# Kernel tuning notes

Hardware: AMD Instinct MI355X
Metric: run time of the kernel (lower is better)

## Reference

```python
import jax, jax.numpy as jnp
import numpy as np

# Static segment boundaries: lengths [512,512,512] + remainder -> ranges below
SEG_RANGES = [(0, 512), (512, 1024), (1024, 1536), (1536, 2048)]

B, N, D, H = 8, 2048, 1024, 2048
NUM_SEG = len(SEG_RANGES)


def setup_inputs() -> dict:
    key = jax.random.key(0)
    k_x, k1, k2, k3 = jax.random.split(key, 4)
    scale_in = 1.0 / np.sqrt(D)
    scale_h = 1.0 / np.sqrt(H)
    return {
        "x": jax.random.normal(k_x, (B, N, D), dtype=jnp.float32),
        "w1": jax.random.normal(k1, (NUM_SEG, D, H), dtype=jnp.float32) * scale_in,
        "w3": jax.random.normal(k2, (NUM_SEG, D, H), dtype=jnp.float32) * scale_in,
        "w2": jax.random.normal(k3, (NUM_SEG, H, D), dtype=jnp.float32) * scale_h,
    }


def reference(x, w1, w3, w2):
    # Per-segment independent SwiGLU FFN: out_seg = (silu(x W1) * (x W3)) W2
    outs = []
    for i, (s, e) in enumerate(SEG_RANGES):
        seg = jax.lax.dynamic_slice_in_dim(x, s, e - s, axis=-2)  # [B, L_i, D]
        h = jax.nn.silu(jnp.einsum('bld,dh->blh', seg, w1[i])) \
            * jnp.einsum('bld,dh->blh', seg, w3[i])               # [B, L_i, H]
        outs.append(jnp.einsum('blh,hd->bld', h, w2[i]))          # [B, L_i, D]
    # Segments tile [0, N) exactly, so concat == the .at[s:e].set() scatter loop
    return jnp.concatenate(outs, axis=-2)
```

## Files before the change

### kernel.cpp

```cpp
#include <hip/hip_runtime.h>
#include <hip/hip_bf16.h>

typedef __bf16 bf16_t;
typedef __attribute__((ext_vector_type(8))) __bf16 bf16x8;
typedef __attribute__((ext_vector_type(4))) float f32x4;
typedef __attribute__((ext_vector_type(8))) unsigned short ushort8v;

#define MFMA16(a, b, c) __builtin_amdgcn_mfma_f32_16x16x32_bf16((a), (b), (c), 0, 0, 0)

__device__ __forceinline__ unsigned short f2bf(float f) {
    bf16_t b = (bf16_t)f;
    return __builtin_bit_cast(unsigned short, b);
}

__device__ __forceinline__ void gload16(const void* g, void* l) {
    __builtin_amdgcn_global_load_lds(
        (const __attribute__((address_space(1))) void*)g,
        (__attribute__((address_space(3))) void*)l,
        16, 0, 0);
}

__global__ __launch_bounds__(256) void cvtx(const float* __restrict__ src,
                                            bf16_t* __restrict__ dst) {
    size_t i = ((size_t)blockIdx.x * 256 + threadIdx.x) * 8;
    f32x4 v0 = *(const f32x4*)(src + i);
    f32x4 v1 = *(const f32x4*)(src + i + 4);
    bf16x8 o;
    o[0] = (bf16_t)v0[0]; o[1] = (bf16_t)v0[1];
    o[2] = (bf16_t)v0[2]; o[3] = (bf16_t)v0[3];
    o[4] = (bf16_t)v1[0]; o[5] = (bf16_t)v1[1];
    o[6] = (bf16_t)v1[2]; o[7] = (bf16_t)v1[3];
    *(bf16x8*)(dst + i) = o;
}

__global__ __launch_bounds__(256) void transcvt64(const float* __restrict__ src,
                                                  unsigned short* __restrict__ dst,
                                                  int R, int C) {
    __shared__ __align__(16) unsigned short tile[64][66];
    size_t off = (size_t)blockIdx.z * R * C;
    const float* s = src + off;
    unsigned short* d = dst + off;
    int tr = blockIdx.y * 64, tc = blockIdx.x * 64;
    int tid = threadIdx.x;
    int lr = tid >> 4;
    int lc = (tid & 15) * 4;
#pragma unroll
    for (int p = 0; p < 4; ++p) {
        int r = p * 16 + lr;
        f32x4 v = *(const f32x4*)(s + (size_t)(tr + r) * C + tc + lc);
        tile[r][lc + 0] = f2bf(v[0]); tile[r][lc + 1] = f2bf(v[1]);
        tile[r][lc + 2] = f2bf(v[2]); tile[r][lc + 3] = f2bf(v[3]);
    }
    __syncthreads();
#pragma unroll
    for (int q = 0; q < 2; ++q) {
        int item = q * 256 + tid;
        int oc = item >> 3;
        int rb = (item & 7) * 8;
        ushort8v v;
#pragma unroll
        for (int t = 0; t < 8; ++t) v[t] = tile[rb + t][oc];
        *(ushort8v*)(d + (size_t)(tc + oc) * R + tr + rb) = v;
    }
}


#define PH_FENCE { __builtin_amdgcn_sched_barrier(0); asm volatile("" ::: "memory"); }
#define LGKM0 { asm volatile("s_waitcnt lgkmcnt(0)" ::: "memory"); __builtin_amdgcn_sched_barrier(0); }

__global__ __launch_bounds__(512, 2) void gemm13(const bf16_t* __restrict__ Xb,
                                                 const bf16_t* __restrict__ W1t,
                                                 const bf16_t* __restrict__ W3t,
                                                 bf16_t* __restrict__ Hh,
                                                 int row_base) {
    const int K = 1024, N = 2048;
    int nwg = gridDim.x, id = blockIdx.x;
    if ((nwg & 7) == 0) id = (id & 7) * (nwg >> 3) + (id >> 3);
    int nbx = nwg >> 4;
    int bx = id % nbx, by = id / nbx;
    int row0 = bx * 256, col0 = by * 128;
    int seg = ((row_base + row0) & 2047) >> 9;
    const bf16_t* Ag  = Xb + (size_t)row0 * K;
    const bf16_t* B1g = W1t + ((size_t)seg * N + col0) * K;
    const bf16_t* B3g = W3t + ((size_t)seg * N + col0) * K;

    __shared__ __align__(16) bf16_t smem[65536];

    int tid = threadIdx.x, lane = tid & 63, w = tid >> 6;
    int wm = w >> 1, wn = w & 1;
    int quad = lane >> 4, l16 = lane & 15;

    int r0 = 2 * (tid >> 3) + ((tid >> 2) & 1);
    int c0 = (tid & 3) ^ ((tid >> 3) & 3);
    int offG  = r0 * K + c0 * 8;
    int offG2 = offG + 128 * K;

    int sigRd = ((l16 & 1) << 2) | (quad ^ ((l16 >> 1) & 3));
    int rdA = (wm * 32 + (l16 >> 1)) * 64 + sigRd * 8;
    int rdB = (wn * 32 + (l16 >> 1)) * 64 + sigRd * 8;

    f32x4 accU[4][4], accV[4][4];
    f32x4 z = {0.f, 0.f, 0.f, 0.f};
#pragma unroll
    for (int i = 0; i < 4; ++i)
#pragma unroll
        for (int j = 0; j < 4; ++j) { accU[i][j] = z; accV[i][j] = z; }

    bf16x8 af[4], bfr[4];

#define STG13(slot, hh) { bf16_t* d_ = smem + (slot) * 16384; const int kg_ = (hh) * 32; \
    gload16(Ag + kg_ + offG,  d_ + tid * 8); \
    gload16(Ag + kg_ + offG2, d_ + 4096 + tid * 8); \
    gload16(B1g + kg_ + offG, d_ + 8192 + tid * 8); \
    gload16(B3g + kg_ + offG, d_ + 12288 + tid * 8); }

#define HALF13(slot, STG, WAIT) {                                               \
    PH_FENCE;                                                                   \
    { const bf16_t* sa_ = smem + (slot) * 16384;                                \
      _Pragma("unroll")                                                         \
      for (int i_ = 0; i_ < 4; ++i_)                                            \
          af[i_] = *(const bf16x8*)(sa_ + rdA + i_ * 512);                      \
      _Pragma("unroll")                                                         \
      for (int j_ = 0; j_ < 4; ++j_)                                            \
          bfr[j_] = *(const bf16x8*)(sa_ + 8192 + rdB + j_ * 512); }            \
    STG;                                                                        \
    __builtin_amdgcn_s_barrier();                                               \
    LGKM0;                                                                      \
    __builtin_amdgcn_s_setprio(1);                                              \
    _Pragma("unroll")                                                           \
    for (int i_ = 0; i_ < 4; ++i_)                                              \
        _Pragma("unroll")                                                       \
        for (int j_ = 0; j_ < 4; ++j_)                                          \
            accU[i_][j_] = MFMA16(af[i_], bfr[j_], accU[i_][j_]);               \
    __builtin_amdgcn_s_setprio(0);                                              \
    __builtin_amdgcn_s_barrier();                                               \
    PH_FENCE;                                                                   \
    { const bf16_t* sb_ = smem + (slot) * 16384 + 12288;                        \
      _Pragma("unroll")                                                         \
      for (int j_ = 0; j_ < 4; ++j_)                                            \
          bfr[j_] = *(const bf16x8*)(sb_ + rdB + j_ * 512); }                   \
    WAIT;                                                                       \
    __builtin_amdgcn_s_barrier();                                               \
    LGKM0;                                                                      \
    __builtin_amdgcn_s_setprio(1);                                              \
    _Pragma("unroll")                                                           \
    for (int i_ = 0; i_ < 4; ++i_)                                              \
        _Pragma("unroll")                                                       \
        for (int j_ = 0; j_ < 4; ++j_)                                          \
            accV[i_][j_] = MFMA16(af[i_], bfr[j_], accV[i_][j_]);               \
    __builtin_amdgcn_s_setprio(0);                                              \
    __builtin_amdgcn_s_barrier(); }

#define W8_13 asm volatile("s_waitcnt vmcnt(8)" ::: "memory")

    STG13(0, 0); STG13(1, 1); STG13(2, 2);
    W8_13;
    __builtin_amdgcn_s_barrier();

#pragma unroll 1
    for (int h = 0; h < 28; h += 4) {
        HALF13(0, STG13(3, h + 3), W8_13);
        HALF13(1, STG13(0, h + 4), W8_13);
        HALF13(2, STG13(1, h + 5), W8_13);
        HALF13(3, STG13(2, h + 6), W8_13);
    }
    HALF13(0, STG13(3, 31), W8_13);
    HALF13(1, , asm volatile("s_waitcnt vmcnt(4)" ::: "memory"));
    HALF13(2, , asm volatile("s_waitcnt vmcnt(0)" ::: "memory"));
    HALF13(3, , );

    __syncthreads();
    bf16_t* Ct = smem;
#pragma unroll
    for (int i = 0; i < 4; ++i)
#pragma unroll
        for (int j = 0; j < 4; ++j) {
            int r = wm * 64 + i * 16 + quad * 4;
            int c = wn * 64 + j * 16 + l16;
#pragma unroll
            for (int t = 0; t < 4; ++t) {
                float u = accU[i][j][t];
                float v = accV[i][j][t];
                float h = (u / (1.f + __expf(-u))) * v;
                Ct[(r + t) * 136 + c] = (bf16_t)h;
            }
        }
    __syncthreads();
#pragma unroll
    for (int s = 0; s < 8; ++s) {
        int r = s * 32 + (tid >> 4);
        int cb = (tid & 15) * 8;
        bf16x8 v = *(const bf16x8*)(Ct + r * 136 + cb);
        *(bf16x8*)(Hh + (size_t)(row0 + r) * N + col0 + cb) = v;
    }
#undef HALF13
#undef STG13
#undef W8_13
}

__global__ __launch_bounds__(512, 2) void gemm2k(const bf16_t* __restrict__ Hh,
                                                 const bf16_t* __restrict__ W2t,
                                                 float* __restrict__ Outc,
                                                 int row_base) {
    const int K = 2048, N = 1024;
    int nwg = gridDim.x, id = blockIdx.x;
    if ((nwg & 7) == 0) id = (id & 7) * (nwg >> 3) + (id >> 3);
    int nbx = nwg >> 2;
    int bx = id % nbx, by = id / nbx;
    int row0 = bx * 256, col0 = by * 256;
    int seg = ((row_base + row0) & 2047) >> 9;
    const bf16_t* Ag = Hh + (size_t)row0 * K;
    const bf16_t* Bg = W2t + ((size_t)seg * N + col0) * K;

    __shared__ __align__(16) bf16_t smem[65536];

    int tid = threadIdx.x, lane = tid & 63, w = tid >> 6;
    int wm = w >> 2, wn = w & 3;
    int quad = lane >> 4, l16 = lane & 15;

    int r0 = 2 * (tid >> 3) + ((tid >> 2) & 1);
    int c0 = (tid & 3) ^ ((tid >> 3) & 3);
    int offG  = r0 * K + c0 * 8;
    int offG2 = offG + 128 * K;

    int sigRd = ((l16 & 1) << 2) | (quad ^ ((l16 >> 1) & 3));
    int rdA = (wm * 64 + (l16 >> 1)) * 64 + sigRd * 8;
    int rdB = (wn * 32 + (l16 >> 1)) * 64 + sigRd * 8;

    f32x4 acc[8][4];
    f32x4 z = {0.f, 0.f, 0.f, 0.f};
#pragma unroll
    for (int i = 0; i < 8; ++i)
#pragma unroll
        for (int j = 0; j < 4; ++j) acc[i][j] = z;

    bf16x8 af[4], bfr[4];

#define STG2(slot, hh) { bf16_t* d_ = smem + (slot) * 16384; const int kg_ = (hh) * 32; \
    gload16(Ag + kg_ + offG,  d_ + tid * 8); \
    gload16(Ag + kg_ + offG2, d_ + 4096 + tid * 8); \
    gload16(Bg + kg_ + offG,  d_ + 8192 + tid * 8); \
    gload16(Bg + kg_ + offG2, d_ + 12288 + tid * 8); }

#define HALF2(slot, STG, WAIT) {                                                \
    PH_FENCE;                                                                   \
    { const bf16_t* s_ = smem + (slot) * 16384;                                 \
      _Pragma("unroll")                                                         \
      for (int i_ = 0; i_ < 4; ++i_)                                            \
          af[i_] = *(const bf16x8*)(s_ + rdA + i_ * 512);                       \
      _Pragma("unroll")                                                         \
      for (int j_ = 0; j_ < 4; ++j_)                                            \
          bfr[j_] = *(const bf16x8*)(s_ + 8192 + rdB + j_ * 512); }             \
    STG;                                                                        \
    __builtin_amdgcn_s_barrier();                                               \
    LGKM0;                                                                      \
    __builtin_amdgcn_s_setprio(1);                                              \
    _Pragma("unroll")                                                           \
    for (int i_ = 0; i_ < 4; ++i_)                                              \
        _Pragma("unroll")                                                       \
        for (int j_ = 0; j_ < 4; ++j_)                                          \
            acc[i_][j_] = MFMA16(af[i_], bfr[j_], acc[i_][j_]);                 \
    __builtin_amdgcn_s_setprio(0);                                              \
    __builtin_amdgcn_s_barrier();                                               \
    PH_FENCE;                                                                   \
    { const bf16_t* s_ = smem + (slot) * 16384;                                 \
      _Pragma("unroll")                                                         \
      for (int i_ = 0; i_ < 4; ++i_)                                            \
          af[i_] = *(const bf16x8*)(s_ + 2048 + rdA + i_ * 512); }              \
    WAIT;                                                                       \
    __builtin_amdgcn_s_barrier();                                               \
    LGKM0;                                                                      \
    __builtin_amdgcn_s_setprio(1);                                              \
    _Pragma("unroll")                                                           \
    for (int i_ = 0; i_ < 4; ++i_)                                              \
        _Pragma("unroll")                                                       \
        for (int j_ = 0; j_ < 4; ++j_)                                          \
            acc[4 + i_][j_] = MFMA16(af[i_], bfr[j_], acc[4 + i_][j_]);         \
    __builtin_amdgcn_s_setprio(0);                                              \
    __builtin_amdgcn_s_barrier(); }

#define W8_2 asm volatile("s_waitcnt vmcnt(8)" ::: "memory")

    STG2(0, 0); STG2(1, 1); STG2(2, 2);
    W8_2;
    __builtin_amdgcn_s_barrier();

#pragma unroll 1
    for (int h = 0; h < 60; h += 4) {
        HALF2(0, STG2(3, h + 3), W8_2);
        HALF2(1, STG2(0, h + 4), W8_2);
        HALF2(2, STG2(1, h + 5), W8_2);
        HALF2(3, STG2(2, h + 6), W8_2);
    }
    HALF2(0, STG2(3, 63), W8_2);
    HALF2(1, , asm volatile("s_waitcnt vmcnt(4)" ::: "memory"));
    HALF2(2, , asm volatile("s_waitcnt vmcnt(0)" ::: "memory"));
    HALF2(3, , );

    __syncthreads();
    float* smemf = (float*)smem;
    for (int pass = 0; pass < 4; ++pass) {
        if (pass) __syncthreads();
        if (wm == (pass >> 1)) {
            int mq = pass & 1;
#pragma unroll
            for (int i = 0; i < 4; ++i)
#pragma unroll
                for (int j = 0; j < 4; ++j) {
                    int r = i * 16 + quad * 4;
                    int c = wn * 64 + j * 16 + l16;
#pragma unroll
                    for (int t = 0; t < 4; ++t)
                        smemf[(r + t) * 260 + c] = acc[mq * 4 + i][j][t];
                }
        }
        __syncthreads();
#pragma unroll
        for (int s = 0; s < 8; ++s) {
            int r = s * 8 + w;
            f32x4 v = *(const f32x4*)(smemf + r * 260 + lane * 4);
            *(f32x4*)(Outc + (size_t)(row0 + pass * 64 + r) * N + col0 + lane * 4) = v;
        }
    }
#undef HALF2
#undef STG2
#undef W8_2
}

extern "C" void kernel_launch(void* const* d_in, const int* in_sizes, int n_in,
                              void* d_out, int out_size, void* d_ws, size_t ws_size,
                              hipStream_t stream) {
    const float* x  = (const float*)d_in[0];
    const float* w1 = (const float*)d_in[1];
    const float* w3 = (const float*)d_in[2];
    const float* w2 = (const float*)d_in[3];
    float* out = (float*)d_out;

    const size_t WSEG = (size_t)4 * 1024 * 2048;
    bf16_t* w1t = (bf16_t*)d_ws;
    bf16_t* w3t = w1t + WSEG;
    bf16_t* w2t = w3t + WSEG;
    bf16_t* dyn = w2t + WSEG;

    transcvt64<<<dim3(32, 16, 4), 256, 0, stream>>>(w1, (unsigned short*)w1t, 1024, 2048);
    transcvt64<<<dim3(32, 16, 4), 256, 0, stream>>>(w3, (unsigned short*)w3t, 1024, 2048);
    transcvt64<<<dim3(16, 32, 4), 256, 0, stream>>>(w2, (unsigned short*)w2t, 2048, 1024);

    const int TOTAL_ROWS = 16384;
    size_t wbytes = 3 * WSEG * sizeof(bf16_t);
    size_t avail = (ws_size > wbytes) ? ws_size - wbytes : 0;
    int chunk_rows = TOTAL_ROWS;
    while (chunk_rows > 256 && (size_t)chunk_rows * 6144 > avail)
        chunk_rows >>= 1;

    for (int rb = 0; rb < TOTAL_ROWS; rb += chunk_rows) {
        bf16_t* Xb = dyn;
        bf16_t* Hh = dyn + (size_t)chunk_rows * 1024;
        cvtx<<<chunk_rows / 2, 256, 0, stream>>>(x + (size_t)rb * 1024, Xb);
        gemm13<<<(chunk_rows / 256) * 16, 512, 0, stream>>>(Xb, w1t, w3t, Hh, rb);
        gemm2k<<<(chunk_rows / 256) * 4, 512, 0, stream>>>(Hh, w2t, out + (size_t)rb * 1024, rb);
    }
}
```

Measured before the change: 397.7 us.

## Issue all LDS fragment reads up front and drop per-half barriers in GEMM loops

In both GEMM kernels, each pipeline stage now issues all twelve fragment reads at once, as inline-asm ds_read_b128 with immediate offsets. It then waits with lgkmcnt(4) before the first MFMA batch and lgkmcnt(0) before the second. The per-half workgroup barriers are collapsed into a single barrier per stage, placed after the vmcnt wait, which removes three barrier round-trips per K-step. The goal is to cut synchronisation stalls and overlap LDS latency with MFMA work. The cost is more live VGPRs for the extra fragment registers, which pressures the 2-waves-per-SIMD occupancy target. Correctness also rests on manual lgkmcnt accounting that the compiler cannot check.

```diff
diff --git a/kernel.cpp b/kernel.cpp
--- a/kernel.cpp
+++ b/kernel.cpp
@@ -7,6 +7,7 @@
 typedef __attribute__((ext_vector_type(8))) unsigned short ushort8v;
 
 #define MFMA16(a, b, c) __builtin_amdgcn_mfma_f32_16x16x32_bf16((a), (b), (c), 0, 0, 0)
+#define BC8(x) __builtin_bit_cast(bf16x8, (x))
 
 __device__ __forceinline__ unsigned short f2bf(float f) {
     bf16_t b = (bf16_t)f;
@@ -65,8 +66,11 @@
 }
 
 
-#define PH_FENCE { __builtin_amdgcn_sched_barrier(0); asm volatile("" ::: "memory"); }
-#define LGKM0 { asm volatile("s_waitcnt lgkmcnt(0)" ::: "memory"); __builtin_amdgcn_sched_barrier(0); }
+#define PH_FENCE __builtin_amdgcn_sched_barrier(0)
+#define LGKMN(n) { asm volatile("s_waitcnt lgkmcnt(" #n ")" ::: "memory"); \
+                   __builtin_amdgcn_sched_barrier(0); }
+#define VMW(n) asm volatile("s_waitcnt vmcnt(" #n ")" ::: "memory")
+#define DSR(dst, a, OFF) asm volatile("ds_read_b128 %0, %1 " OFF : "=v"(dst) : "v"(a))
 
 __global__ __launch_bounds__(512, 2) void gemm13(const bf16_t* __restrict__ Xb,
                                                  const bf16_t* __restrict__ W1t,
@@ -96,8 +100,8 @@
     int offG2 = offG + 128 * K;
 
     int sigRd = ((l16 & 1) << 2) | (quad ^ ((l16 >> 1) & 3));
-    int rdA = (wm * 32 + (l16 >> 1)) * 64 + sigRd * 8;
-    int rdB = (wn * 32 + (l16 >> 1)) * 64 + sigRd * 8;
+    int rdAB = ((wm * 32 + (l16 >> 1)) * 64 + sigRd * 8) * 2;
+    int rdBB = ((wn * 32 + (l16 >> 1)) * 64 + sigRd * 8) * 2;
 
     f32x4 accU[4][4], accV[4][4];
     f32x4 z = {0.f, 0.f, 0.f, 0.f};
@@ -106,7 +110,7 @@
 #pragma unroll
         for (int j = 0; j < 4; ++j) { accU[i][j] = z; accV[i][j] = z; }
 
-    bf16x8 af[4], bfr[4];
+    f32x4 af[4], bU[4], bV[4];
 
 #define STG13(slot, hh) { bf16_t* d_ = smem + (slot) * 16384; const int kg_ = (hh) * 32; \
     gload16(Ag + kg_ + offG,  d_ + tid * 8); \
@@ -116,57 +120,48 @@
 
 #define HALF13(slot, STG, WAIT) {                                               \
     PH_FENCE;                                                                   \
-    { const bf16_t* sa_ = smem + (slot) * 16384;                                \
-      _Pragma("unroll")                                                         \
-      for (int i_ = 0; i_ < 4; ++i_)                                            \
-          af[i_] = *(const bf16x8*)(sa_ + rdA + i_ * 512);                      \
-      _Pragma("unroll")                                                         \
-      for (int j_ = 0; j_ < 4; ++j_)                                            \
-          bfr[j_] = *(const bf16x8*)(sa_ + 8192 + rdB + j_ * 512); }            \
     STG;                                                                        \
-    __builtin_amdgcn_s_barrier();                                               \
-    LGKM0;                                                                      \
+    int aA_ = (slot) * 32768 + rdAB;                                            \
+    int aB_ = (slot) * 32768 + rdBB;                                            \
+    DSR(af[0], aA_, "offset:0");     DSR(af[1], aA_, "offset:1024");            \
+    DSR(af[2], aA_, "offset:2048");  DSR(af[3], aA_, "offset:3072");            \
+    DSR(bU[0], aB_, "offset:16384"); DSR(bU[1], aB_, "offset:17408");           \
+    DSR(bU[2], aB_, "offset:18432"); DSR(bU[3], aB_, "offset:19456");           \
+    DSR(bV[0], aB_, "offset:24576"); DSR(bV[1], aB_, "offset:25600");           \
+    DSR(bV[2], aB_, "offset:26624"); DSR(bV[3], aB_, "offset:27648");           \
+    LGKMN(4);                                                                   \
     __builtin_amdgcn_s_setprio(1);                                              \
     _Pragma("unroll")                                                           \
     for (int i_ = 0; i_ < 4; ++i_)                                              \
         _Pragma("unroll")                                                       \
         for (int j_ = 0; j_ < 4; ++j_)                                          \
-            accU[i_][j_] = MFMA16(af[i_], bfr[j_], accU[i_][j_]);               \
+            accU[i_][j_] = MFMA16(BC8(af[i_]), BC8(bU[j_]), accU[i_][j_]);      \
     __builtin_amdgcn_s_setprio(0);                                              \
-    __builtin_amdgcn_s_barrier();                                               \
-    PH_FENCE;                                                                   \
-    { const bf16_t* sb_ = smem + (slot) * 16384 + 12288;                        \
-      _Pragma("unroll")                                                         \
-      for (int j_ = 0; j_ < 4; ++j_)                                            \
-          bfr[j_] = *(const bf16x8*)(sb_ + rdB + j_ * 512); }                   \
-    WAIT;                                                                       \
-    __builtin_amdgcn_s_barrier();                                               \
-    LGKM0;                                                                      \
+    LGKMN(0);                                                                   \
     __builtin_amdgcn_s_setprio(1);                                              \
     _Pragma("unroll")                                                           \
     for (int i_ = 0; i_ < 4; ++i_)                                              \
         _Pragma("unroll")                                                       \
         for (int j_ = 0; j_ < 4; ++j_)                                          \
-            accV[i_][j_] = MFMA16(af[i_], bfr[j_], accV[i_][j_]);               \
+            accV[i_][j_] = MFMA16(BC8(af[i_]), BC8(bV[j_]), accV[i_][j_]);      \
     __builtin_amdgcn_s_setprio(0);                                              \
+    WAIT;                                                                       \
     __builtin_amdgcn_s_barrier(); }
 
-#define W8_13 asm volatile("s_waitcnt vmcnt(8)" ::: "memory")
-
     STG13(0, 0); STG13(1, 1); STG13(2, 2);
-    W8_13;
+    VMW(8);
     __builtin_amdgcn_s_barrier();
 
 #pragma unroll 1
     for (int h = 0; h < 28; h += 4) {
-        HALF13(0, STG13(3, h + 3), W8_13);
-        HALF13(1, STG13(0, h + 4), W8_13);
-        HALF13(2, STG13(1, h + 5), W8_13);
-        HALF13(3, STG13(2, h + 6), W8_13);
-    }
-    HALF13(0, STG13(3, 31), W8_13);
-    HALF13(1, , asm volatile("s_waitcnt vmcnt(4)" ::: "memory"));
-    HALF13(2, , asm volatile("s_waitcnt vmcnt(0)" ::: "memory"));
+        HALF13(0, STG13(3, h + 3), VMW(8));
+        HALF13(1, STG13(0, h + 4), VMW(8));
+        HALF13(2, STG13(1, h + 5), VMW(8));
+        HALF13(3, STG13(2, h + 6), VMW(8));
+    }
+    HALF13(0, STG13(3, 31), VMW(8));
+    HALF13(1, , VMW(4));
+    HALF13(2, , VMW(0));
     HALF13(3, , );
 
     __syncthreads();
@@ -195,7 +190,6 @@
     }
 #undef HALF13
 #undef STG13
-#undef W8_13
 }
 
 __global__ __launch_bounds__(512, 2) void gemm2k(const bf16_t* __restrict__ Hh,
@@ -224,8 +218,8 @@
     int offG2 = offG + 128 * K;
 
     int sigRd = ((l16 & 1) << 2) | (quad ^ ((l16 >> 1) & 3));
-    int rdA = (wm * 64 + (l16 >> 1)) * 64 + sigRd * 8;
-    int rdB = (wn * 32 + (l16 >> 1)) * 64 + sigRd * 8;
+    int rdAB = ((wm * 64 + (l16 >> 1)) * 64 + sigRd * 8) * 2;
+    int rdBB = ((wn * 32 + (l16 >> 1)) * 64 + sigRd * 8) * 2;
 
     f32x4 acc[8][4];
     f32x4 z = {0.f, 0.f, 0.f, 0.f};
@@ -234,7 +228,7 @@
 #pragma unroll
         for (int j = 0; j < 4; ++j) acc[i][j] = z;
 
-    bf16x8 af[4], bfr[4];
+    f32x4 af[4], ag[4], bfr[4];
 
 #define STG2(slot, hh) { bf16_t* d_ = smem + (slot) * 16384; const int kg_ = (hh) * 32; \
     gload16(Ag + kg_ + offG,  d_ + tid * 8); \
@@ -244,57 +238,48 @@
 
 #define HALF2(slot, STG, WAIT) {                                                \
     PH_FENCE;                                                                   \
-    { const bf16_t* s_ = smem + (slot) * 16384;                                 \
-      _Pragma("unroll")                                                         \
-      for (int i_ = 0; i_ < 4; ++i_)                                            \
-          af[i_] = *(const bf16x8*)(s_ + rdA + i_ * 512);                       \
-      _Pragma("unroll")                                                         \
-      for (int j_ = 0; j_ < 4; ++j_)                                            \
-          bfr[j_] = *(const bf16x8*)(s_ + 8192 + rdB + j_ * 512); }             \
     STG;                                                                        \
-    __builtin_amdgcn_s_barrier();                                               \
-    LGKM0;                                                                      \
+    int aA_ = (slot) * 32768 + rdAB;                                            \
+    int aB_ = (slot) * 32768 + rdBB;                                            \
+    DSR(af[0], aA_, "offset:0");      DSR(af[1], aA_, "offset:1024");           \
+    DSR(af[2], aA_, "offset:2048");   DSR(af[3], aA_, "offset:3072");           \
+    DSR(bfr[0], aB_, "offset:16384"); DSR(bfr[1], aB_, "offset:17408");         \
+    DSR(bfr[2], aB_, "offset:18432"); DSR(bfr[3], aB_, "offset:19456");         \
+    DSR(ag[0], aA_, "offset:4096");   DSR(ag[1], aA_, "offset:5120");           \
+    DSR(ag[2], aA_, "offset:6144");   DSR(ag[3], aA_, "offset:7168");           \
+    LGKMN(4);                                                                   \
     __builtin_amdgcn_s_setprio(1);                                              \
     _Pragma("unroll")                                                           \
     for (int i_ = 0; i_ < 4; ++i_)                                              \
         _Pragma("unroll")                                                       \
         for (int j_ = 0; j_ < 4; ++j_)                                          \
-            acc[i_][j_] = MFMA16(af[i_], bfr[j_], acc[i_][j_]);                 \
+            acc[i_][j_] = MFMA16(BC8(af[i_]), BC8(bfr[j_]), acc[i_][j_]);       \
     __builtin_amdgcn_s_setprio(0);                                              \
-    __builtin_amdgcn_s_barrier();                                               \
-    PH_FENCE;                                                                   \
-    { const bf16_t* s_ = smem + (slot) * 16384;                                 \
-      _Pragma("unroll")                                                         \
-      for (int i_ = 0; i_ < 4; ++i_)                                            \
-          af[i_] = *(const bf16x8*)(s_ + 2048 + rdA + i_ * 512); }              \
-    WAIT;                                                                       \
-    __builtin_amdgcn_s_barrier();                                               \
-    LGKM0;                                                                      \
+    LGKMN(0);                                                                   \
     __builtin_amdgcn_s_setprio(1);                                              \
     _Pragma("unroll")                                                           \
     for (int i_ = 0; i_ < 4; ++i_)                                              \
         _Pragma("unroll")                                                       \
         for (int j_ = 0; j_ < 4; ++j_)                                          \
-            acc[4 + i_][j_] = MFMA16(af[i_], bfr[j_], acc[4 + i_][j_]);         \
+            acc[4 + i_][j_] = MFMA16(BC8(ag[i_]), BC8(bfr[j_]), acc[4 + i_][j_]); \
     __builtin_amdgcn_s_setprio(0);                                              \
+    WAIT;                                                                       \
     __builtin_amdgcn_s_barrier(); }
 
-#define W8_2 asm volatile("s_waitcnt vmcnt(8)" ::: "memory")
-
     STG2(0, 0); STG2(1, 1); STG2(2, 2);
-    W8_2;
+    VMW(8);
     __builtin_amdgcn_s_barrier();
 
 #pragma unroll 1
     for (int h = 0; h < 60; h += 4) {
-        HALF2(0, STG2(3, h + 3), W8_2);
-        HALF2(1, STG2(0, h + 4), W8_2);
-        HALF2(2, STG2(1, h + 5), W8_2);
-        HALF2(3, STG2(2, h + 6), W8_2);
-    }
-    HALF2(0, STG2(3, 63), W8_2);
-    HALF2(1, , asm volatile("s_waitcnt vmcnt(4)" ::: "memory"));
-    HALF2(2, , asm volatile("s_waitcnt vmcnt(0)" ::: "memory"));
+        HALF2(0, STG2(3, h + 3), VMW(8));
+        HALF2(1, STG2(0, h + 4), VMW(8));
+        HALF2(2, STG2(1, h + 5), VMW(8));
+        HALF2(3, STG2(2, h + 6), VMW(8));
+    }
+    HALF2(0, STG2(3, 63), VMW(8));
+    HALF2(1, , VMW(4));
+    HALF2(2, , VMW(0));
     HALF2(3, , );
 
     __syncthreads();
@@ -324,7 +309,6 @@
     }
 #undef HALF2
 #undef STG2
-#undef W8_2
 }
 
 extern "C" void kernel_launch(void* const* d_in, const int* in_sizes, int n_in,
```

New measurement: 400.3 us. About the same (+0.7%).
